# Performance work log

Hardware: AMD Instinct MI355X
Metric: run time of the kernel (lower is better)

The kernel has to match this reference:

```python
import jax, jax.numpy as jnp
import numpy as np

CUTOFF = 10.0
EPS_W = 1e-5
EPS_LN = 1e-5

def _silu(v):
    return v * jax.nn.sigmoid(v)

def setup_inputs() -> dict:
    key = jax.random.key(0)
    ks = jax.random.split(key, 12)
    N, E, H, R = 50000, 300000, 256, 64
    s = lambda fan_in: 1.0 / np.sqrt(fan_in)
    inp = {
        'x': jax.random.normal(ks[0], (N, H), jnp.float32),
        'edge_index': jax.random.randint(ks[1], (2, E), 0, N, jnp.int64 if jax.config.jax_enable_x64 else jnp.int32),
        'distances': jax.random.uniform(ks[2], (E,), jnp.float32) * CUTOFF,
        'centers': jnp.linspace(0.0, CUTOFF, R).astype(jnp.float32),
        'widths': jnp.full((R,), CUTOFF / R, jnp.float32),
        'rbf_w1': jax.random.normal(ks[3], (R, R), jnp.float32) * s(R),
        'rbf_b1': jnp.zeros((R,), jnp.float32),
        'rbf_w2': jax.random.normal(ks[4], (R, R), jnp.float32) * s(R),
        'rbf_b2': jnp.zeros((R,), jnp.float32),
        'filt_w1': jax.random.normal(ks[5], (R, H), jnp.float32) * s(R),
        'filt_b1': jnp.zeros((H,), jnp.float32),
        'filt_w2': jax.random.normal(ks[6], (H, H), jnp.float32) * s(H),
        'filt_b2': jnp.zeros((H,), jnp.float32),
        'filt_w3': jax.random.normal(ks[7], (H, H), jnp.float32) * s(H),
        'filt_b3': jnp.zeros((H,), jnp.float32),
        'node_w': jax.random.normal(ks[8], (H, H), jnp.float32) * s(H),
        'node_b': jnp.zeros((H,), jnp.float32),
        'ln_g': jnp.ones((H,), jnp.float32),
        'ln_b': jnp.zeros((H,), jnp.float32),
        'gate_w': jax.random.normal(ks[9], (H, H), jnp.float32) * s(H),
        'gate_b': jnp.zeros((H,), jnp.float32),
    }
    return inp

def reference(x, edge_index, distances, centers, widths,
              rbf_w1, rbf_b1, rbf_w2, rbf_b2,
              filt_w1, filt_b1, filt_w2, filt_b2, filt_w3, filt_b3,
              node_w, node_b, ln_g, ln_b, gate_w, gate_b):
    # LearnableRBF: envelope * gaussian basis, then 2-layer SiLU proj
    d = distances
    env = 0.5 * (jnp.cos(d * jnp.pi / CUTOFF) + 1.0) * (d < CUTOFF).astype(x.dtype)  # [E]
    rbf = jnp.exp(-0.5 * ((d[:, None] - centers) / (jnp.abs(widths) + EPS_W)) ** 2)   # [E,R]
    r = rbf * env[:, None]
    r = _silu(r @ rbf_w1 + rbf_b1) @ rbf_w2 + rbf_b2                                  # [E,R]
    # filter network: Lin-SiLU-Lin-SiLU-Lin
    W = _silu(r @ filt_w1 + filt_b1)
    W = _silu(W @ filt_w2 + filt_b2) @ filt_w3 + filt_b3                              # [E,H]
    # gather -> modulate -> scatter-add (CFConv messaging)
    row, col = edge_index[0], edge_index[1]
    msg = (x[col] @ node_w + node_b) * W                                              # [E,H]
    agg = jax.ops.segment_sum(msg, row, num_segments=x.shape[0])                      # [N,H]
    h = x + agg
    mu = jnp.mean(h, axis=-1, keepdims=True)
    var = jnp.var(h, axis=-1, keepdims=True)
    out = (h - mu) / jnp.sqrt(var + EPS_LN) * ln_g + ln_b
    return out * jax.nn.sigmoid(out @ gate_w + gate_b)
```

## Files before the change

kernel.cpp:

```cpp
#include <hip/hip_runtime.h>
#include <hip/hip_bf16.h>
#include <math.h>

typedef __attribute__((ext_vector_type(8))) short bf16x8;
typedef __attribute__((ext_vector_type(4))) float f32x4;
typedef unsigned short ushort_t;

constexpr float F_CUTOFF = 10.0f;
constexpr float F_EPS_W  = 1e-5f;
constexpr float F_EPS_LN = 1e-5f;
constexpr float F_PI     = 3.14159265358979323846f;

__device__ __forceinline__ float silu_f(float v)   { return v / (1.0f + __expf(-v)); }
__device__ __forceinline__ float sigmoid_f(float v){ return 1.0f / (1.0f + __expf(-v)); }

__device__ __forceinline__ ushort_t f2bf(float f) {
    union { __hip_bfloat16 h; ushort_t u; } v; v.h = __float2bfloat16(f); return v.u;
}
__device__ __forceinline__ float bf2f(ushort_t u) {
    union { __hip_bfloat16 h; ushort_t u; } v; v.u = u; return __bfloat162float(v.h);
}

__device__ __forceinline__ float f4c(const float4& v, int q) {
    return q == 0 ? v.x : q == 1 ? v.y : q == 2 ? v.z : v.w;
}

__global__ void cvt_transpose_kernel(const float* __restrict__ in, ushort_t* __restrict__ out,
                                     int K, int N, int logK)
{
    int idx = blockIdx.x * 256 + threadIdx.x;
    if (idx >= K * N) return;
    int n = idx >> logK;
    int k = idx & (K - 1);
    out[idx] = f2bf(in[k * N + n]);
}

__global__ void combine_w_kernel(const float* __restrict__ w2, const float* __restrict__ fw1,
                                 ushort_t* __restrict__ out)
{
    int idx = blockIdx.x * 256 + threadIdx.x;
    int c = idx >> 6, j = idx & 63;
    float s = 0.f;
    #pragma unroll 8
    for (int n = 0; n < 64; ++n) s += w2[j * 64 + n] * fw1[n * 256 + c];
    out[idx] = f2bf(s);
}

__global__ void combine_b_kernel(const float* __restrict__ b2, const float* __restrict__ fw1,
                                 const float* __restrict__ fb1, float* __restrict__ out)
{
    int c = threadIdx.x;
    float s = fb1[c];
    #pragma unroll 8
    for (int n = 0; n < 64; ++n) s += b2[n] * fw1[n * 256 + c];
    out[c] = s;
}

__global__ __launch_bounds__(256)
void gemm256_bf16_kernel(const float* __restrict__ A, const float* __restrict__ Wm,
                         const float* __restrict__ bias, ushort_t* __restrict__ out, int M)
{
    __shared__ float4 As4[64][64];
    const int t = threadIdx.x;
    const int row0 = blockIdx.x * 64;

    #pragma unroll
    for (int i = 0; i < 16; ++i) {
        int flat = t + i * 256;
        int r = flat >> 6, k4 = flat & 63;
        int row = row0 + r;
        float4 v = make_float4(0.f, 0.f, 0.f, 0.f);
        if (row < M) v = reinterpret_cast<const float4*>(A)[row * 64 + k4];
        As4[r][k4] = v;
    }
    __syncthreads();

    const int jt  = t & 31;
    const int et  = t >> 5;
    const int j04 = jt * 2;
    const int r0  = et * 8;

    float acc[8][8];
    #pragma unroll
    for (int r = 0; r < 8; ++r)
        #pragma unroll
        for (int c = 0; c < 8; ++c) acc[r][c] = 0.f;

    for (int k4 = 0; k4 < 64; ++k4) {
        float4 a4[8];
        #pragma unroll
        for (int r = 0; r < 8; ++r) a4[r] = As4[r0 + r][k4];
        #pragma unroll
        for (int q = 0; q < 4; ++q) {
            const int k = k4 * 4 + q;
            float4 b0 = reinterpret_cast<const float4*>(Wm)[k * 64 + j04];
            float4 b1 = reinterpret_cast<const float4*>(Wm)[k * 64 + j04 + 1];
            float bb[8] = {b0.x, b0.y, b0.z, b0.w, b1.x, b1.y, b1.z, b1.w};
            #pragma unroll
            for (int r = 0; r < 8; ++r) {
                float av = f4c(a4[r], q);
                #pragma unroll
                for (int c = 0; c < 8; ++c) acc[r][c] = fmaf(av, bb[c], acc[r][c]);
            }
        }
    }

    float4 bv0 = reinterpret_cast<const float4*>(bias)[j04];
    float4 bv1 = reinterpret_cast<const float4*>(bias)[j04 + 1];
    float bb[8] = {bv0.x, bv0.y, bv0.z, bv0.w, bv1.x, bv1.y, bv1.z, bv1.w};

    #pragma unroll
    for (int r = 0; r < 8; ++r) {
        int row = row0 + r0 + r;
        if (row >= M) continue;
        ushort_t o8[8];
        #pragma unroll
        for (int c = 0; c < 8; ++c) o8[c] = f2bf(acc[r][c] + bb[c]);
        *reinterpret_cast<uint4*>(out + (size_t)row * 256 + jt * 8) = *reinterpret_cast<uint4*>(o8);
    }
}

__global__ __launch_bounds__(256)
void gate_gemm_kernel(const float* __restrict__ A, const float* __restrict__ Wm,
                      const float* __restrict__ bias, float* __restrict__ out, int M)
{
    __shared__ float4 As4[64][64];
    const int t = threadIdx.x;
    const int row0 = blockIdx.x * 64;

    #pragma unroll
    for (int i = 0; i < 16; ++i) {
        int flat = t + i * 256;
        int r = flat >> 6, k4 = flat & 63;
        int row = row0 + r;
        float4 v = make_float4(0.f, 0.f, 0.f, 0.f);
        if (row < M) v = reinterpret_cast<const float4*>(A)[row * 64 + k4];
        As4[r][k4] = v;
    }
    __syncthreads();

    const int jt  = t & 31;
    const int et  = t >> 5;
    const int j04 = jt * 2;
    const int r0  = et * 8;

    float acc[8][8];
    #pragma unroll
    for (int r = 0; r < 8; ++r)
        #pragma unroll
        for (int c = 0; c < 8; ++c) acc[r][c] = 0.f;

    for (int k4 = 0; k4 < 64; ++k4) {
        float4 a4[8];
        #pragma unroll
        for (int r = 0; r < 8; ++r) a4[r] = As4[r0 + r][k4];
        #pragma unroll
        for (int q = 0; q < 4; ++q) {
            const int k = k4 * 4 + q;
            float4 b0 = reinterpret_cast<const float4*>(Wm)[k * 64 + j04];
            float4 b1 = reinterpret_cast<const float4*>(Wm)[k * 64 + j04 + 1];
            float bb[8] = {b0.x, b0.y, b0.z, b0.w, b1.x, b1.y, b1.z, b1.w};
            #pragma unroll
            for (int r = 0; r < 8; ++r) {
                float av = f4c(a4[r], q);
                #pragma unroll
                for (int c = 0; c < 8; ++c) acc[r][c] = fmaf(av, bb[c], acc[r][c]);
            }
        }
    }

    float4 bv0 = reinterpret_cast<const float4*>(bias)[j04];
    float4 bv1 = reinterpret_cast<const float4*>(bias)[j04 + 1];
    float bb[8] = {bv0.x, bv0.y, bv0.z, bv0.w, bv1.x, bv1.y, bv1.z, bv1.w};

    #pragma unroll
    for (int r = 0; r < 8; ++r) {
        int row = row0 + r0 + r;
        if (row >= M) continue;
        float4 a0 = As4[r0 + r][j04];
        float4 a1 = As4[r0 + r][j04 + 1];
        float aa[8] = {a0.x, a0.y, a0.z, a0.w, a1.x, a1.y, a1.z, a1.w};
        float o[8];
        #pragma unroll
        for (int c = 0; c < 8; ++c) o[c] = aa[c] * sigmoid_f(acc[r][c] + bb[c]);
        reinterpret_cast<float4*>(out)[row * 64 + j04]     = make_float4(o[0], o[1], o[2], o[3]);
        reinterpret_cast<float4*>(out)[row * 64 + j04 + 1] = make_float4(o[4], o[5], o[6], o[7]);
    }
}

template<int KS, int NT, bool SILU>
__device__ __forceinline__ void mlp_stage(const unsigned char* in, unsigned char* out,
                                          const ushort_t* __restrict__ Wt,
                                          const float* __restrict__ bias,
                                          int wm, int wn, int g, int q)
{
    constexpr int K = KS * 32;
    f32x4 acc[2][NT];
    #pragma unroll
    for (int mt = 0; mt < 2; ++mt)
        #pragma unroll
        for (int nt = 0; nt < NT; ++nt) acc[mt][nt] = (f32x4){0.f, 0.f, 0.f, 0.f};

    #pragma unroll
    for (int kk = 0; kk < KS; ++kk) {
        bf16x8 b[NT];
        #pragma unroll
        for (int nt = 0; nt < NT; ++nt) {
            int n = (wn * NT + nt) * 16 + q;
            b[nt] = *reinterpret_cast<const bf16x8*>(Wt + n * K + kk * 32 + g * 8);
        }
        bf16x8 a[2];
        #pragma unroll
        for (int mt = 0; mt < 2; ++mt) {
            int m = wm * 32 + mt * 16 + q;
            int unit = (4 * kk + g) ^ (m & 7);
            a[mt] = *reinterpret_cast<const bf16x8*>(in + m * 512 + unit * 16);
        }
        #pragma unroll
        for (int mt = 0; mt < 2; ++mt)
            #pragma unroll
            for (int nt = 0; nt < NT; ++nt)
                acc[mt][nt] = __builtin_amdgcn_mfma_f32_16x16x32_bf16(a[mt], b[nt], acc[mt][nt], 0, 0, 0);
    }

    const bool evenq = (q & 1) == 0;
    #pragma unroll
    for (int nt = 0; nt < NT; ++nt) {
        int n0  = (wn * NT + nt) * 16 + q;
        int n_e = n0 & ~1;
        float2 bv = *reinterpret_cast<const float2*>(bias + n_e);
        #pragma unroll
        for (int mt = 0; mt < 2; ++mt) {
            float v[4], p[4];
            #pragma unroll
            for (int r = 0; r < 4; ++r) { v[r] = acc[mt][nt][r]; p[r] = __shfl_xor(v[r], 1, 64); }
            #pragma unroll
            for (int rr = 0; rr < 2; ++rr) {
                int r = evenq ? rr : (2 + rr);
                float lo = (evenq ? v[r] : p[r]) + bv.x;
                float hi = (evenq ? p[r] : v[r]) + bv.y;
                if (SILU) { lo = silu_f(lo); hi = silu_f(hi); }
                int m = wm * 32 + mt * 16 + 4 * g + r;
                unsigned u = (unsigned)f2bf(lo) | ((unsigned)f2bf(hi) << 16);
                int byte = m * 512 + (((n_e >> 3) ^ (m & 7)) << 4) + ((n_e & 7) * 2);
                *reinterpret_cast<unsigned*>(out + byte) = u;
            }
        }
    }
}

__global__ __launch_bounds__(512, 4)
void edge_mfma_kernel(const float* __restrict__ dist, const int* __restrict__ eidx,
                      const float* __restrict__ centers, const float* __restrict__ widths,
                      const ushort_t* __restrict__ wt_rbf1, const float* __restrict__ rbf_b1,
                      const ushort_t* __restrict__ wt_comb, const float* __restrict__ b_comb,
                      const ushort_t* __restrict__ wt_f2, const float* __restrict__ filt_b2,
                      const ushort_t* __restrict__ wt_f3, const float* __restrict__ filt_b3,
                      const ushort_t* __restrict__ y, float* __restrict__ agg, int E)
{
    __shared__ __align__(16) unsigned char bufA[32768];
    __shared__ __align__(16) unsigned char bufB[32768];

    const int t  = threadIdx.x;
    const int e0 = blockIdx.x * 64;
    const int w    = t >> 6;
    const int wm   = w >> 2, wn = w & 3;
    const int lane = t & 63;
    const int g = lane >> 4, q = lane & 15;

    {
        int e  = t >> 3;
        int k0 = (t & 7) * 8;
        int ge = e0 + e;
        float d = (ge < E) ? dist[ge] : F_CUTOFF;
        float env = (d < F_CUTOFF) ? 0.5f * (__cosf(d * (F_PI / F_CUTOFF)) + 1.0f) : 0.0f;
        unsigned char* rowp = bufA + e * 512;
        #pragma unroll
        for (int i = 0; i < 4; ++i) {
            int n = k0 + 2 * i;
            float c0 = centers[n],     w0 = fabsf(widths[n]) + F_EPS_W;
            float c1 = centers[n + 1], w1 = fabsf(widths[n + 1]) + F_EPS_W;
            float z0 = (d - c0) / w0, z1 = (d - c1) / w1;
            float r0 = env * __expf(-0.5f * z0 * z0);
            float r1 = env * __expf(-0.5f * z1 * z1);
            unsigned u = (unsigned)f2bf(r0) | ((unsigned)f2bf(r1) << 16);
            int byte = (((n >> 3) ^ (e & 7)) << 4) + ((n & 7) * 2);
            *reinterpret_cast<unsigned*>(rowp + byte) = u;
        }
    }
    __syncthreads();

    mlp_stage<2, 1, true>(bufA, bufB, wt_rbf1, rbf_b1, wm, wn, g, q);
    __syncthreads();
    mlp_stage<2, 4, true>(bufB, bufA, wt_comb, b_comb, wm, wn, g, q);
    __syncthreads();
    mlp_stage<8, 4, true>(bufA, bufB, wt_f2, filt_b2, wm, wn, g, q);
    __syncthreads();

    {
        f32x4 acc[2][4];
        #pragma unroll
        for (int mt = 0; mt < 2; ++mt)
            #pragma unroll
            for (int nt = 0; nt < 4; ++nt) acc[mt][nt] = (f32x4){0.f, 0.f, 0.f, 0.f};

        #pragma unroll
        for (int kk = 0; kk < 8; ++kk) {
            bf16x8 b[4];
            #pragma unroll
            for (int nt = 0; nt < 4; ++nt) {
                int n = (wn * 4 + nt) * 16 + q;
                b[nt] = *reinterpret_cast<const bf16x8*>(wt_f3 + n * 256 + kk * 32 + g * 8);
            }
            bf16x8 a[2];
            #pragma unroll
            for (int mt = 0; mt < 2; ++mt) {
                int m = wm * 32 + mt * 16 + q;
                int unit = (4 * kk + g) ^ (m & 7);
                a[mt] = *reinterpret_cast<const bf16x8*>(bufB + m * 512 + unit * 16);
            }
            #pragma unroll
            for (int mt = 0; mt < 2; ++mt)
                #pragma unroll
                for (int nt = 0; nt < 4; ++nt)
                    acc[mt][nt] = __builtin_amdgcn_mfma_f32_16x16x32_bf16(a[mt], b[nt], acc[mt][nt], 0, 0, 0);
        }

        float bn[4];
        int   nn[4];
        #pragma unroll
        for (int nt = 0; nt < 4; ++nt) { nn[nt] = (wn * 4 + nt) * 16 + q; bn[nt] = filt_b3[nn[nt]]; }

        #pragma unroll
        for (int mt = 0; mt < 2; ++mt) {
            #pragma unroll
            for (int r = 0; r < 4; ++r) {
                int m  = wm * 32 + mt * 16 + 4 * g + r;
                int ge = e0 + m;
                if (ge < E) {
                    int rowi = eidx[ge];
                    int coli = eidx[E + ge];
                    const ushort_t* yrow = y + (size_t)coli * 256;
                    float* arow = agg + (size_t)rowi * 256;
                    #pragma unroll
                    for (int nt = 0; nt < 4; ++nt) {
                        float wv = acc[mt][nt][r] + bn[nt];
                        float yv = bf2f(yrow[nn[nt]]);
                        unsafeAtomicAdd(&arow[nn[nt]], wv * yv);
                    }
                }
            }
        }
    }
}

__global__ __launch_bounds__(256)
void ln_kernel(const float* __restrict__ x, const float* __restrict__ agg,
               const float* __restrict__ g, const float* __restrict__ b,
               float* __restrict__ out0, int N)
{
    int lane = threadIdx.x & 63;
    int row  = blockIdx.x * 4 + (threadIdx.x >> 6);
    if (row >= N) return;
    float4 hx = reinterpret_cast<const float4*>(x)[row * 64 + lane];
    float4 ha = reinterpret_cast<const float4*>(agg)[row * 64 + lane];
    float4 h  = make_float4(hx.x + ha.x, hx.y + ha.y, hx.z + ha.z, hx.w + ha.w);
    float s  = h.x + h.y + h.z + h.w;
    float s2 = h.x * h.x + h.y * h.y + h.z * h.z + h.w * h.w;
    #pragma unroll
    for (int off = 32; off > 0; off >>= 1) {
        s  += __shfl_xor(s,  off, 64);
        s2 += __shfl_xor(s2, off, 64);
    }
    float mu  = s * (1.0f / 256.0f);
    float var = s2 * (1.0f / 256.0f) - mu * mu;
    float inv = rsqrtf(var + F_EPS_LN);
    float4 gv = reinterpret_cast<const float4*>(g)[lane];
    float4 bv = reinterpret_cast<const float4*>(b)[lane];
    float4 o;
    o.x = (h.x - mu) * inv * gv.x + bv.x;
    o.y = (h.y - mu) * inv * gv.y + bv.y;
    o.z = (h.z - mu) * inv * gv.z + bv.z;
    o.w = (h.w - mu) * inv * gv.w + bv.w;
    reinterpret_cast<float4*>(out0)[row * 64 + lane] = o;
}

extern "C" void kernel_launch(void* const* d_in, const int* in_sizes, int n_in,
                              void* d_out, int out_size, void* d_ws, size_t ws_size,
                              hipStream_t stream)
{
    const float* x       = (const float*)d_in[0];
    const int*   eidx    = (const int*)  d_in[1];
    const float* dist    = (const float*)d_in[2];
    const float* centers = (const float*)d_in[3];
    const float* widths  = (const float*)d_in[4];
    const float* rbf_w1  = (const float*)d_in[5];
    const float* rbf_b1  = (const float*)d_in[6];
    const float* rbf_w2  = (const float*)d_in[7];
    const float* rbf_b2  = (const float*)d_in[8];
    const float* filt_w1 = (const float*)d_in[9];
    const float* filt_b1 = (const float*)d_in[10];
    const float* filt_w2 = (const float*)d_in[11];
    const float* filt_b2 = (const float*)d_in[12];
    const float* filt_w3 = (const float*)d_in[13];
    const float* filt_b3 = (const float*)d_in[14];
    const float* node_w  = (const float*)d_in[15];
    const float* node_b  = (const float*)d_in[16];
    const float* ln_g    = (const float*)d_in[17];
    const float* ln_b    = (const float*)d_in[18];
    const float* gate_w  = (const float*)d_in[19];
    const float* gate_b  = (const float*)d_in[20];

    const int N = in_sizes[0] / 256;
    const int E = in_sizes[2];

    ushort_t* y_bf   = (ushort_t*)d_ws;
    ushort_t* wt1    = y_bf + (size_t)N * 256;
    ushort_t* wcomb  = wt1 + 64 * 64;
    ushort_t* wf2    = wcomb + 256 * 64;
    ushort_t* wf3    = wf2 + 256 * 256;
    float*    bcomb  = (float*)(wf3 + 256 * 256);

    float* agg = (float*)d_out;

    hipMemsetAsync(d_out, 0, (size_t)out_size * sizeof(float), stream);

    cvt_transpose_kernel<<<dim3((64 * 64 + 255) / 256),   256, 0, stream>>>(rbf_w1,  wt1, 64, 64, 6);
    combine_w_kernel<<<dim3(64), 256, 0, stream>>>(rbf_w2, filt_w1, wcomb);
    combine_b_kernel<<<dim3(1), 256, 0, stream>>>(rbf_b2, filt_w1, filt_b1, bcomb);
    cvt_transpose_kernel<<<dim3((256 * 256 + 255) / 256), 256, 0, stream>>>(filt_w2, wf2, 256, 256, 8);
    cvt_transpose_kernel<<<dim3((256 * 256 + 255) / 256), 256, 0, stream>>>(filt_w3, wf3, 256, 256, 8);

    gemm256_bf16_kernel<<<dim3((N + 63) / 64), 256, 0, stream>>>(x, node_w, node_b, y_bf, N);

    edge_mfma_kernel<<<dim3((E + 63) / 64), 512, 0, stream>>>(
        dist, eidx, centers, widths,
        wt1, rbf_b1, wcomb, bcomb,
        wf2, filt_b2, wf3, filt_b3,
        y_bf, agg, E);

    ln_kernel<<<dim3((N + 3) / 4), 256, 0, stream>>>(x, agg, ln_g, ln_b, (float*)d_out, N);
    gate_gemm_kernel<<<dim3((N + 63) / 64), 256, 0, stream>>>((float*)d_out, gate_w, gate_b, (float*)d_out, N);
}
```

Measured before the change: 848.0 us.

## Halve edge tile and prefetch gathered node rows into LDS early

```diff
diff --git a/kernel.cpp b/kernel.cpp
--- a/kernel.cpp
+++ b/kernel.cpp
@@ -192,7 +192,7 @@
 __device__ __forceinline__ void mlp_stage(const unsigned char* in, unsigned char* out,
                                           const ushort_t* __restrict__ Wt,
                                           const float* __restrict__ bias,
-                                          int wm, int wn, int g, int q)
+                                          int wn, int g, int q)
 {
     constexpr int K = KS * 32;
     f32x4 acc[2][NT];
@@ -212,7 +212,7 @@
         bf16x8 a[2];
         #pragma unroll
         for (int mt = 0; mt < 2; ++mt) {
-            int m = wm * 32 + mt * 16 + q;
+            int m = mt * 16 + q;
             int unit = (4 * kk + g) ^ (m & 7);
             a[mt] = *reinterpret_cast<const bf16x8*>(in + m * 512 + unit * 16);
         }
@@ -240,7 +240,7 @@
                 float lo = (evenq ? v[r] : p[r]) + bv.x;
                 float hi = (evenq ? p[r] : v[r]) + bv.y;
                 if (SILU) { lo = silu_f(lo); hi = silu_f(hi); }
-                int m = wm * 32 + mt * 16 + 4 * g + r;
+                int m = mt * 16 + 4 * g + r;
                 unsigned u = (unsigned)f2bf(lo) | ((unsigned)f2bf(hi) << 16);
                 int byte = m * 512 + (((n_e >> 3) ^ (m & 7)) << 4) + ((n_e & 7) * 2);
                 *reinterpret_cast<unsigned*>(out + byte) = u;
@@ -249,7 +249,7 @@
     }
 }
 
-__global__ __launch_bounds__(512, 4)
+__global__ __launch_bounds__(256, 4)
 void edge_mfma_kernel(const float* __restrict__ dist, const int* __restrict__ eidx,
                       const float* __restrict__ centers, const float* __restrict__ widths,
                       const ushort_t* __restrict__ wt_rbf1, const float* __restrict__ rbf_b1,
@@ -258,23 +258,29 @@
                       const ushort_t* __restrict__ wt_f3, const float* __restrict__ filt_b3,
                       const ushort_t* __restrict__ y, float* __restrict__ agg, int E)
 {
-    __shared__ __align__(16) unsigned char bufA[32768];
-    __shared__ __align__(16) unsigned char bufB[32768];
+    __shared__ __align__(16) unsigned char bufA[16384];
+    __shared__ __align__(16) unsigned char bufB[16384];
 
     const int t  = threadIdx.x;
-    const int e0 = blockIdx.x * 64;
-    const int w    = t >> 6;
-    const int wm   = w >> 2, wn = w & 3;
+    const int e0 = blockIdx.x * 32;
+    const int wn   = t >> 6;
     const int lane = t & 63;
     const int g = lane >> 4, q = lane & 15;
 
+    const int e_own  = t >> 3;
+    const int chunk  = t & 7;
+    const int ge_own = e0 + e_own;
+    const int col_own = (ge_own < E) ? eidx[E + ge_own] : 0;
+    uint4 yv[4];
+    #pragma unroll
+    for (int i = 0; i < 4; ++i)
+        yv[i] = *reinterpret_cast<const uint4*>(y + (size_t)col_own * 256 + (i * 8 + chunk) * 8);
+
     {
-        int e  = t >> 3;
-        int k0 = (t & 7) * 8;
-        int ge = e0 + e;
-        float d = (ge < E) ? dist[ge] : F_CUTOFF;
+        float d = (ge_own < E) ? dist[ge_own] : F_CUTOFF;
         float env = (d < F_CUTOFF) ? 0.5f * (__cosf(d * (F_PI / F_CUTOFF)) + 1.0f) : 0.0f;
-        unsigned char* rowp = bufA + e * 512;
+        unsigned char* rowp = bufA + e_own * 512;
+        int k0 = chunk * 8;
         #pragma unroll
         for (int i = 0; i < 4; ++i) {
             int n = k0 + 2 * i;
@@ -284,17 +290,22 @@
             float r0 = env * __expf(-0.5f * z0 * z0);
             float r1 = env * __expf(-0.5f * z1 * z1);
             unsigned u = (unsigned)f2bf(r0) | ((unsigned)f2bf(r1) << 16);
-            int byte = (((n >> 3) ^ (e & 7)) << 4) + ((n & 7) * 2);
+            int byte = (((n >> 3) ^ (e_own & 7)) << 4) + ((n & 7) * 2);
             *reinterpret_cast<unsigned*>(rowp + byte) = u;
         }
     }
     __syncthreads();
 
-    mlp_stage<2, 1, true>(bufA, bufB, wt_rbf1, rbf_b1, wm, wn, g, q);
-    __syncthreads();
-    mlp_stage<2, 4, true>(bufB, bufA, wt_comb, b_comb, wm, wn, g, q);
-    __syncthreads();
-    mlp_stage<8, 4, true>(bufA, bufB, wt_f2, filt_b2, wm, wn, g, q);
+    mlp_stage<2, 1, true>(bufA, bufB, wt_rbf1, rbf_b1, wn, g, q);
+    __syncthreads();
+    mlp_stage<2, 4, true>(bufB, bufA, wt_comb, b_comb, wn, g, q);
+    __syncthreads();
+    mlp_stage<8, 4, true>(bufA, bufB, wt_f2, filt_b2, wn, g, q);
+    __syncthreads();
+
+    #pragma unroll
+    for (int i = 0; i < 4; ++i)
+        *reinterpret_cast<uint4*>(bufA + e_own * 512 + (i * 8 + chunk) * 16) = yv[i];
     __syncthreads();
 
     {
@@ -315,7 +326,7 @@
             bf16x8 a[2];
             #pragma unroll
             for (int mt = 0; mt < 2; ++mt) {
-                int m = wm * 32 + mt * 16 + q;
+                int m = mt * 16 + q;
                 int unit = (4 * kk + g) ^ (m & 7);
                 a[mt] = *reinterpret_cast<const bf16x8*>(bufB + m * 512 + unit * 16);
             }
@@ -335,18 +346,17 @@
         for (int mt = 0; mt < 2; ++mt) {
             #pragma unroll
             for (int r = 0; r < 4; ++r) {
-                int m  = wm * 32 + mt * 16 + 4 * g + r;
+                int m  = mt * 16 + 4 * g + r;
                 int ge = e0 + m;
                 if (ge < E) {
                     int rowi = eidx[ge];
-                    int coli = eidx[E + ge];
-                    const ushort_t* yrow = y + (size_t)coli * 256;
                     float* arow = agg + (size_t)rowi * 256;
+                    const unsigned char* yrow = bufA + m * 512;
                     #pragma unroll
                     for (int nt = 0; nt < 4; ++nt) {
                         float wv = acc[mt][nt][r] + bn[nt];
-                        float yv = bf2f(yrow[nn[nt]]);
-                        unsafeAtomicAdd(&arow[nn[nt]], wv * yv);
+                        float yvv = bf2f(*reinterpret_cast<const ushort_t*>(yrow + nn[nt] * 2));
+                        unsafeAtomicAdd(&arow[nn[nt]], wv * yvv);
                     }
                 }
             }
@@ -433,7 +443,7 @@
 
     gemm256_bf16_kernel<<<dim3((N + 63) / 64), 256, 0, stream>>>(x, node_w, node_b, y_bf, N);
 
-    edge_mfma_kernel<<<dim3((E + 63) / 64), 512, 0, stream>>>(
+    edge_mfma_kernel<<<dim3((E + 31) / 32), 256, 0, stream>>>(
         dist, eidx, centers, widths,
         wt1, rbf_b1, wcomb, bcomb,
         wf2, filt_b2, wf3, filt_b3,
```

Measured after the change: 824.4 us. 2.8% less time.
